# Optimization experiments

Hardware: AMD Instinct MI355X
Metric: run time of the kernel (lower is better)

The kernel has to match this reference:

```python
import jax, jax.numpy as jnp
import numpy as np

N_EMBD = 2048
N_HEAD = 16
HEAD_DIM = N_EMBD // N_HEAD
B, T = 4, 2048
EPS = 1e-5


def layer_norm(x, w, b):
    mu = jnp.mean(x, axis=-1, keepdims=True)
    var = jnp.var(x, axis=-1, keepdims=True)
    return (x - mu) * jax.lax.rsqrt(var + EPS) * w + b


def setup_inputs() -> dict:
    key = jax.random.key(0)
    ks = jax.random.split(key, 8)
    s = 0.02
    return {
        "x": jax.random.normal(ks[0], (B, T, N_EMBD), dtype=jnp.float32),
        "ln1_w": jnp.ones((N_EMBD,), jnp.float32),
        "ln1_b": jnp.zeros((N_EMBD,), jnp.float32),
        "attn_w": jax.random.normal(ks[1], (N_EMBD, 3 * N_EMBD), jnp.float32) * s,
        "attn_b": jnp.zeros((3 * N_EMBD,), jnp.float32),
        "ln2_w": jnp.ones((N_EMBD,), jnp.float32),
        "ln2_b": jnp.zeros((N_EMBD,), jnp.float32),
        "fc_w": jax.random.normal(ks[2], (N_EMBD, 4 * N_EMBD), jnp.float32) * s,
        "fc_b": jnp.zeros((4 * N_EMBD,), jnp.float32),
        "proj_w": jax.random.normal(ks[3], (4 * N_EMBD, N_EMBD), jnp.float32) * s,
        "proj_b": jnp.zeros((N_EMBD,), jnp.float32),
    }


def reference(x, ln1_w, ln1_b, attn_w, attn_b, ln2_w, ln2_b, fc_w, fc_b, proj_w, proj_b):
    b, t, c = x.shape
    # --- causal self-attention on ln_1(x); note: source Block has NO residual
    # and attention's c_proj is never invoked in the original forward. ---
    h = layer_norm(x, ln1_w, ln1_b)
    qkv = h @ attn_w + attn_b                      # [B,T,3C]
    q, k, v = jnp.split(qkv, 3, axis=-1)
    q = q.reshape(b, t, N_HEAD, HEAD_DIM)
    k = k.reshape(b, t, N_HEAD, HEAD_DIM)
    v = v.reshape(b, t, N_HEAD, HEAD_DIM)
    scale = 1.0 / np.sqrt(HEAD_DIM).astype(np.float32)
    scores = jnp.einsum("bqhd,bkhd->bhqk", q, k) * scale   # [B,H,T,T]
    causal = jnp.tril(jnp.ones((t, t), dtype=bool))
    scores = jnp.where(causal, scores, -jnp.inf)
    attn = jax.nn.softmax(scores, axis=-1)
    y = jnp.einsum("bhqk,bkhd->bqhd", attn, v).reshape(b, t, c)
    # --- MLP on ln_2(y); again no residual in the source Block ---
    h2 = layer_norm(y, ln2_w, ln2_b)
    out = jax.nn.gelu(h2 @ fc_w + fc_b, approximate=False) @ proj_w + proj_b
    return out
```

## Files before the change

kernel.cpp:

```cpp
#include <hip/hip_runtime.h>
#include <hip/hip_bf16.h>

typedef __attribute__((ext_vector_type(8))) short      bf16x8;
typedef __attribute__((ext_vector_type(4))) float      f32x4;
typedef __attribute__((ext_vector_type(8))) unsigned short u16x8;

__device__ __forceinline__ unsigned short f2bf(float f) {
    union { __hip_bfloat16 h; unsigned short u; } cv;
    cv.h = __float2bfloat16(f);
    return cv.u;
}
__device__ __forceinline__ float bf2f(unsigned short u) {
    union { float f; unsigned int i; } cv;
    cv.i = ((unsigned int)u) << 16;
    return cv.f;
}
__device__ __forceinline__ void gload_lds16(const void* g, void* l) {
    __builtin_amdgcn_global_load_lds(
        (const __attribute__((address_space(1))) void*)g,
        (__attribute__((address_space(3))) void*)l, 16, 0, 0);
}
__device__ __forceinline__ f32x4 mfma16(bf16x8 a, bf16x8 b, f32x4 c) {
    return __builtin_amdgcn_mfma_f32_16x16x32_bf16(a, b, c, 0, 0, 0);
}
__device__ __forceinline__ float gelu_f(float x) {
    return 0.5f * x * (1.0f + erff(x * 0.70710678118654752f));
}

#define S_BARRIER() asm volatile("s_barrier" ::: "memory")
#define LGKM0()     do { asm volatile("s_waitcnt lgkmcnt(0)" ::: "memory"); \
                         __builtin_amdgcn_sched_barrier(0); } while (0)

template<int IN_BF16>
__global__ __launch_bounds__(256) void ln_kernel(const void* in, const float* w, const float* b,
                                                 unsigned short* out) {
    const int row = blockIdx.x;
    const int tid = threadIdx.x;
    float v[8];
    if constexpr (IN_BF16) {
        const unsigned short* p = (const unsigned short*)in + (size_t)row * 2048 + tid * 8;
        u16x8 raw = *(const u16x8*)p;
#pragma unroll
        for (int j = 0; j < 8; j++) v[j] = bf2f(raw[j]);
    } else {
        const float* p = (const float*)in + (size_t)row * 2048 + tid * 8;
        float4 a = ((const float4*)p)[0];
        float4 c = ((const float4*)p)[1];
        v[0] = a.x; v[1] = a.y; v[2] = a.z; v[3] = a.w;
        v[4] = c.x; v[5] = c.y; v[6] = c.z; v[7] = c.w;
    }
    float s = 0.f, ss = 0.f;
#pragma unroll
    for (int j = 0; j < 8; j++) { s += v[j]; ss += v[j] * v[j]; }
#pragma unroll
    for (int off = 32; off > 0; off >>= 1) {
        s  += __shfl_xor(s, off);
        ss += __shfl_xor(ss, off);
    }
    __shared__ float red[8];
    const int wid = tid >> 6, lane = tid & 63;
    if (lane == 0) { red[wid] = s; red[4 + wid] = ss; }
    __syncthreads();
    s  = red[0] + red[1] + red[2] + red[3];
    ss = red[4] + red[5] + red[6] + red[7];
    const float mean = s * (1.0f / 2048.0f);
    const float var  = ss * (1.0f / 2048.0f) - mean * mean;
    const float rstd = rsqrtf(var + 1e-5f);
    unsigned short* op = out + (size_t)row * 2048 + tid * 8;
    u16x8 ov;
#pragma unroll
    for (int j = 0; j < 8; j++) {
        int c = tid * 8 + j;
        ov[j] = f2bf((v[j] - mean) * rstd * w[c] + b[c]);
    }
    *(u16x8*)op = ov;
}

__global__ __launch_bounds__(256) void wt_kernel(const float* W, unsigned short* WT, int K, int N) {
    __shared__ unsigned short sm[32][33];
    const int n0 = blockIdx.x * 32, k0 = blockIdx.y * 32;
    const int tx = threadIdx.x, ty = threadIdx.y;
#pragma unroll
    for (int i = 0; i < 4; i++) {
        int k = ty + i * 8;
        sm[k][tx] = f2bf(W[(size_t)(k0 + k) * N + n0 + tx]);
    }
    __syncthreads();
#pragma unroll
    for (int i = 0; i < 4; i++) {
        int n = ty + i * 8;
        WT[(size_t)(n0 + n) * K + k0 + tx] = sm[tx][n];
    }
}

__global__ __launch_bounds__(256) void vt_kernel(const unsigned short* qkv, unsigned short* vT) {
    __shared__ unsigned short sm[32][33];
    const int t0 = blockIdx.x * 32, d0 = blockIdx.y * 32, bh = blockIdx.z;
    const int b = bh >> 4, h = bh & 15;
    const int tx = threadIdx.x, ty = threadIdx.y;
#pragma unroll
    for (int i = 0; i < 4; i++) {
        int t = ty + i * 8;
        sm[t][tx] = qkv[(size_t)(b * 2048 + t0 + t) * 6144 + 4096 + h * 128 + d0 + tx];
    }
    __syncthreads();
#pragma unroll
    for (int i = 0; i < 4; i++) {
        int d = ty + i * 8;
        vT[(size_t)(bh * 128 + d0 + d) * 2048 + t0 + tx] = sm[tx][d];
    }
}

template<int OUT_BF16, int ACT_GELU>
__global__ __launch_bounds__(512, 2) void gemm256(const unsigned short* __restrict__ A,
                                                  const unsigned short* __restrict__ BT,
                                                  const float* __restrict__ bias,
                                                  void* __restrict__ Cout,
                                                  int M, int N, int K) {
    __shared__ unsigned short As[2][256 * 64];
    __shared__ unsigned short Bs[2][256 * 64];
    const int tid = threadIdx.x;
    const int gx = gridDim.x;
    const int lin = blockIdx.y * gx + blockIdx.x;
    const int cpx = (gx * gridDim.y) >> 3;
    const int swz = (lin & 7) * cpx + (lin >> 3);
    const int n0 = (swz % gx) * 256, m0 = (swz / gx) * 256;

    const int wid = tid >> 6, lane = tid & 63;
    const int wr = wid >> 2, wc = wid & 3;
    const int lg = lane >> 4, l15 = lane & 15;
    const int nkt = K >> 6;

    const int sr = tid >> 3;
    const int scol = ((tid & 7) ^ (sr & 7)) * 8;
    const int sdst = tid * 8;

    auto stageA = [&](int ta, int h) {
        const unsigned short* g = A + (size_t)(m0 + h * 128 + sr) * K + ta * 64 + scol;
        unsigned short* d = &As[ta & 1][h * 8192 + sdst];
        gload_lds16(g, d);
        gload_lds16(g + (size_t)64 * K, d + 4096);
    };
    auto stageB = [&](int ta, int h) {
        const unsigned short* g = BT + (size_t)(n0 + h * 128 + sr) * K + ta * 64 + scol;
        unsigned short* d = &Bs[ta & 1][h * 8192 + sdst];
        gload_lds16(g, d);
        gload_lds16(g + (size_t)64 * K, d + 4096);
    };

    stageA(0, 0); stageA(0, 1); stageB(0, 0); stageB(0, 1);
    if (nkt > 1) {
        stageA(1, 0); stageA(1, 1);
        asm volatile("s_waitcnt vmcnt(4)" ::: "memory");
    } else {
        asm volatile("s_waitcnt vmcnt(0)" ::: "memory");
    }
    S_BARRIER();

    f32x4 acc[8][4] = {};
    const int lxor = l15 & 7;
    const int co0 = (lg ^ lxor) * 8;
    const int co1 = ((4 + lg) ^ lxor) * 8;
    const int arow = wr * 128 + l15;
    const int brow = wc * 64 + l15;

    for (int t = 0; t < nkt; ++t) {
        const int p = t & 1;
        const unsigned short* Ap = As[p];
        const unsigned short* Bp = Bs[p];
        bf16x8 af0[8], af1[8], bq0, bq1;

#pragma unroll
        for (int m = 0; m < 8; m++) {
            const int rb = (arow + m * 16) * 64;
            af0[m] = *(const bf16x8*)&Ap[rb + co0];
            af1[m] = *(const bf16x8*)&Ap[rb + co1];
        }
        bq0 = *(const bf16x8*)&Bp[(brow) * 64 + co0];
        bq1 = *(const bf16x8*)&Bp[(brow + 16) * 64 + co0];
        if (t + 1 < nkt) { stageB(t + 1, 0); stageB(t + 1, 1); }
        S_BARRIER();
        LGKM0();
        __builtin_amdgcn_s_setprio(1);
#pragma unroll
        for (int m = 0; m < 8; m++) {
            acc[m][0] = mfma16(af0[m], bq0, acc[m][0]);
            acc[m][1] = mfma16(af0[m], bq1, acc[m][1]);
        }
        __builtin_amdgcn_s_setprio(0);
        S_BARRIER();

        bq0 = *(const bf16x8*)&Bp[(brow + 32) * 64 + co0];
        bq1 = *(const bf16x8*)&Bp[(brow + 48) * 64 + co0];
        if (t + 2 < nkt) stageA(t + 2, 0);
        S_BARRIER();
        LGKM0();
        __builtin_amdgcn_s_setprio(1);
#pragma unroll
        for (int m = 0; m < 8; m++) {
            acc[m][2] = mfma16(af0[m], bq0, acc[m][2]);
            acc[m][3] = mfma16(af0[m], bq1, acc[m][3]);
        }
        __builtin_amdgcn_s_setprio(0);
        S_BARRIER();

        bq0 = *(const bf16x8*)&Bp[(brow) * 64 + co1];
        bq1 = *(const bf16x8*)&Bp[(brow + 16) * 64 + co1];
        if (t + 2 < nkt) stageA(t + 2, 1);
        S_BARRIER();
        LGKM0();
        __builtin_amdgcn_s_setprio(1);
#pragma unroll
        for (int m = 0; m < 8; m++) {
            acc[m][0] = mfma16(af1[m], bq0, acc[m][0]);
            acc[m][1] = mfma16(af1[m], bq1, acc[m][1]);
        }
        __builtin_amdgcn_s_setprio(0);
        S_BARRIER();

        bq0 = *(const bf16x8*)&Bp[(brow + 32) * 64 + co1];
        bq1 = *(const bf16x8*)&Bp[(brow + 48) * 64 + co1];
        S_BARRIER();
        LGKM0();
        __builtin_amdgcn_s_setprio(1);
#pragma unroll
        for (int m = 0; m < 8; m++) {
            acc[m][2] = mfma16(af1[m], bq0, acc[m][2]);
            acc[m][3] = mfma16(af1[m], bq1, acc[m][3]);
        }
        __builtin_amdgcn_s_setprio(0);
        if (t + 2 < nkt)      asm volatile("s_waitcnt vmcnt(4)" ::: "memory");
        else if (t + 1 < nkt) asm volatile("s_waitcnt vmcnt(0)" ::: "memory");
        S_BARRIER();
    }

#pragma unroll
    for (int n = 0; n < 4; n++) {
        const int col = n0 + wc * 64 + n * 16 + l15;
        const float bv = bias[col];
#pragma unroll
        for (int m = 0; m < 8; m++) {
            const int rbase = m0 + wr * 128 + m * 16 + lg * 4;
#pragma unroll
            for (int r = 0; r < 4; r++) {
                float v = acc[m][n][r] + bv;
                if (ACT_GELU) v = gelu_f(v);
                if (OUT_BF16)
                    ((unsigned short*)Cout)[(size_t)(rbase + r) * N + col] = f2bf(v);
                else
                    ((float*)Cout)[(size_t)(rbase + r) * N + col] = v;
            }
        }
    }
}

__global__ __launch_bounds__(256) void attn_kernel(const unsigned short* __restrict__ qkv,
                                                   const unsigned short* __restrict__ vT,
                                                   unsigned short* __restrict__ y) {
    __shared__ unsigned short Qs[64 * 128];
    __shared__ unsigned short Ks[64 * 128];
    __shared__ unsigned short VTs[128 * 64];
    const int pair = blockIdx.x, h = blockIdx.y, b = blockIdx.z;
    const int tid = threadIdx.x, wid = tid >> 6, lane = tid & 63;
    const int lg = lane >> 4, l15 = lane & 15;
    const float scale = 0.08838834764831845f;
    unsigned short* Ps = &Qs[wid * 1024];

    for (int pass = 0; pass < 2; pass++) {
        const int qt = (pass == 0) ? (31 - pair) : pair;
        __syncthreads();
#pragma unroll
        for (int i = 0; i < 4; i++) {
            int idx = tid + 256 * i;
            int row = idx >> 4, ch = idx & 15;
            const unsigned short* g = qkv + (size_t)(b * 2048 + qt * 64 + row) * 6144
                                      + h * 128 + ((ch ^ (row & 7)) * 8);
            gload_lds16(g, &Qs[idx * 8]);
        }
        __syncthreads();
        const int rq = wid * 16 + l15;
        bf16x8 qf[4];
#pragma unroll
        for (int c = 0; c < 4; c++)
            qf[c] = *(const bf16x8*)&Qs[rq * 128 + (((c * 4 + lg) ^ (rq & 7)) * 8)];

        float m_run[4], l_run[4];
#pragma unroll
        for (int r = 0; r < 4; r++) { m_run[r] = -1e30f; l_run[r] = 0.f; }
        f32x4 O[8] = {};

        const int nkb = qt + 1;
        for (int kb = 0; kb < nkb; kb++) {
            __syncthreads();
#pragma unroll
            for (int i = 0; i < 4; i++) {
                int idx = tid + 256 * i;
                int row = idx >> 4, ch = idx & 15;
                const unsigned short* g = qkv + (size_t)(b * 2048 + kb * 64 + row) * 6144
                                          + 2048 + h * 128 + ((ch ^ (row & 7)) * 8);
                gload_lds16(g, &Ks[idx * 8]);
            }
#pragma unroll
            for (int i = 0; i < 4; i++) {
                int idx = tid + 256 * i;
                int row = idx >> 3, ch = idx & 7;
                const unsigned short* g = vT + (size_t)((b * 16 + h) * 128 + row) * 2048
                                          + kb * 64 + ((ch ^ (row & 7)) * 8);
                gload_lds16(g, &VTs[idx * 8]);
            }
            __syncthreads();

            f32x4 S[4] = {};
#pragma unroll
            for (int n = 0; n < 4; n++) {
                const int rk = n * 16 + l15;
#pragma unroll
                for (int c = 0; c < 4; c++) {
                    bf16x8 kf = *(const bf16x8*)&Ks[rk * 128 + (((c * 4 + lg) ^ (rk & 7)) * 8)];
                    S[n] = mfma16(qf[c], kf, S[n]);
                }
            }

            const int qgb = qt * 64 + wid * 16 + lg * 4;
#pragma unroll
            for (int r = 0; r < 4; r++) {
                const int qg = qgb + r;
                float sv[4];
#pragma unroll
                for (int n = 0; n < 4; n++) {
                    const int kg = kb * 64 + n * 16 + l15;
                    sv[n] = (kg <= qg) ? S[n][r] * scale : -1e30f;
                }
                float mx = fmaxf(fmaxf(sv[0], sv[1]), fmaxf(sv[2], sv[3]));
                mx = fmaxf(mx, __shfl_xor(mx, 1));
                mx = fmaxf(mx, __shfl_xor(mx, 2));
                mx = fmaxf(mx, __shfl_xor(mx, 4));
                mx = fmaxf(mx, __shfl_xor(mx, 8));
                const float mnew = fmaxf(m_run[r], mx);
                const float f = __expf(m_run[r] - mnew);
                const float p0 = __expf(sv[0] - mnew), p1 = __expf(sv[1] - mnew);
                const float p2 = __expf(sv[2] - mnew), p3 = __expf(sv[3] - mnew);
                float rs = (p0 + p1) + (p2 + p3);
                rs += __shfl_xor(rs, 1);
                rs += __shfl_xor(rs, 2);
                rs += __shfl_xor(rs, 4);
                rs += __shfl_xor(rs, 8);
                l_run[r] = l_run[r] * f + rs;
                m_run[r] = mnew;
#pragma unroll
                for (int n2 = 0; n2 < 8; n2++) O[n2][r] *= f;
                const int prow = lg * 4 + r;
                const int pxor = (prow & 7) << 3;
                Ps[(prow * 64 + l15) ^ pxor]      = f2bf(p0);
                Ps[(prow * 64 + 16 + l15) ^ pxor] = f2bf(p1);
                Ps[(prow * 64 + 32 + l15) ^ pxor] = f2bf(p2);
                Ps[(prow * 64 + 48 + l15) ^ pxor] = f2bf(p3);
            }

#pragma unroll
            for (int kk = 0; kk < 2; kk++) {
                bf16x8 pf = *(const bf16x8*)&Ps[l15 * 64 + (((kk * 4 + lg) ^ (l15 & 7)) * 8)];
#pragma unroll
                for (int n2 = 0; n2 < 8; n2++) {
                    const int rv = n2 * 16 + l15;
                    bf16x8 vf = *(const bf16x8*)&VTs[rv * 64 + (((kk * 4 + lg) ^ (rv & 7)) * 8)];
                    O[n2] = mfma16(pf, vf, O[n2]);
                }
            }
        }

#pragma unroll
        for (int r = 0; r < 4; r++) {
            const float inv = 1.0f / l_run[r];
            const size_t row = (size_t)(b * 2048 + qt * 64 + wid * 16 + lg * 4 + r);
#pragma unroll
            for (int n2 = 0; n2 < 8; n2++)
                y[row * 2048 + h * 128 + n2 * 16 + l15] = f2bf(O[n2][r] * inv);
        }
    }
}

extern "C" void kernel_launch(void* const* d_in, const int* in_sizes, int n_in,
                              void* d_out, int out_size, void* d_ws, size_t ws_size,
                              hipStream_t stream) {
    const float* x      = (const float*)d_in[0];
    const float* ln1_w  = (const float*)d_in[1];
    const float* ln1_b  = (const float*)d_in[2];
    const float* attn_w = (const float*)d_in[3];
    const float* attn_b = (const float*)d_in[4];
    const float* ln2_w  = (const float*)d_in[5];
    const float* ln2_b  = (const float*)d_in[6];
    const float* fc_w   = (const float*)d_in[7];
    const float* fc_b   = (const float*)d_in[8];
    const float* proj_w = (const float*)d_in[9];
    const float* proj_b = (const float*)d_in[10];
    float* out = (float*)d_out;

    char* ws = (char*)d_ws;
    const size_t MB = 1024ull * 1024ull;
    unsigned short* Wt   = (unsigned short*)(ws + 0);
    unsigned short* X1   = (unsigned short*)(ws + 32 * MB);
    unsigned short* X2   = (unsigned short*)(ws + 64 * MB);
    unsigned short* QKV  = (unsigned short*)(ws + 96 * MB);
    unsigned short* VT   = (unsigned short*)(ws + 192 * MB);
    unsigned short* Abuf = (unsigned short*)(ws + 96 * MB);

    ln_kernel<0><<<8192, 256, 0, stream>>>(x, ln1_w, ln1_b, X1);
    wt_kernel<<<dim3(6144 / 32, 2048 / 32), dim3(32, 8), 0, stream>>>(attn_w, Wt, 2048, 6144);
    gemm256<1, 0><<<dim3(24, 32), 512, 0, stream>>>(X1, Wt, attn_b, QKV, 8192, 6144, 2048);
    vt_kernel<<<dim3(64, 4, 64), dim3(32, 8), 0, stream>>>(QKV, VT);
    attn_kernel<<<dim3(16, 16, 4), 256, 0, stream>>>(QKV, VT, X2);
    ln_kernel<1><<<8192, 256, 0, stream>>>(X2, ln2_w, ln2_b, X1);
    wt_kernel<<<dim3(8192 / 32, 2048 / 32), dim3(32, 8), 0, stream>>>(fc_w, Wt, 2048, 8192);
    gemm256<1, 1><<<dim3(32, 32), 512, 0, stream>>>(X1, Wt, fc_b, Abuf, 8192, 8192, 2048);
    wt_kernel<<<dim3(2048 / 32, 8192 / 32), dim3(32, 8), 0, stream>>>(proj_w, Wt, 8192, 2048);
    gemm256<0, 0><<<dim3(8, 32), 512, 0, stream>>>(Abuf, Wt, proj_b, out, 8192, 2048, 8192);
}
```

Measured before the change: 1.045 ms.

## Restructure GEMM main loop into four half-M phases with one-tile-ahead prefetch

Rewrites the GEMM K-loop as four macro-generated phases. Each phase loads four A fragments and four B fragments and issues a 4x4 block of MFMAs, instead of holding all eight A fragments per K-half across the whole iteration. A and B are now both prefetched only one tile ahead, and the loop waits for all loads with vmcnt(0) at the end of each iteration. This is meant to cut register pressure and simplify the schedule, at the cost of a shallower prefetch that may expose more global-load latency.

After: 1.062 ms. Within noise of the previous version (+1.6%).

```diff
diff --git a/kernel.cpp b/kernel.cpp
--- a/kernel.cpp
+++ b/kernel.cpp
@@ -149,12 +149,7 @@
     };
 
     stageA(0, 0); stageA(0, 1); stageB(0, 0); stageB(0, 1);
-    if (nkt > 1) {
-        stageA(1, 0); stageA(1, 1);
-        asm volatile("s_waitcnt vmcnt(4)" ::: "memory");
-    } else {
-        asm volatile("s_waitcnt vmcnt(0)" ::: "memory");
-    }
+    asm volatile("s_waitcnt vmcnt(0)" ::: "memory");
     S_BARRIER();
 
     f32x4 acc[8][4] = {};
@@ -164,75 +159,49 @@
     const int arow = wr * 128 + l15;
     const int brow = wc * 64 + l15;
 
+#define GPHASE(MH, CO, READB, STAGE_STMT, TAIL_STMT)                              \
+    do {                                                                          \
+        bf16x8 af[4];                                                             \
+        _Pragma("unroll")                                                         \
+        for (int i = 0; i < 4; i++)                                               \
+            af[i] = *(const bf16x8*)&Ap[(arow + ((MH) * 4 + i) * 16) * 64 + (CO)];\
+        if (READB) {                                                              \
+            _Pragma("unroll")                                                     \
+            for (int n = 0; n < 4; n++)                                           \
+                bq[n] = *(const bf16x8*)&Bp[(brow + n * 16) * 64 + (CO)];         \
+        }                                                                         \
+        STAGE_STMT;                                                               \
+        S_BARRIER();                                                              \
+        LGKM0();                                                                  \
+        __builtin_amdgcn_s_setprio(1);                                            \
+        _Pragma("unroll")                                                         \
+        for (int i = 0; i < 4; i++) {                                             \
+            _Pragma("unroll")                                                     \
+            for (int n = 0; n < 4; n++)                                           \
+                acc[(MH) * 4 + i][n] = mfma16(af[i], bq[n], acc[(MH) * 4 + i][n]);\
+        }                                                                         \
+        __builtin_amdgcn_s_setprio(0);                                            \
+        TAIL_STMT;                                                                \
+        S_BARRIER();                                                              \
+    } while (0)
+
     for (int t = 0; t < nkt; ++t) {
         const int p = t & 1;
         const unsigned short* Ap = As[p];
         const unsigned short* Bp = Bs[p];
-        bf16x8 af0[8], af1[8], bq0, bq1;
-
-#pragma unroll
-        for (int m = 0; m < 8; m++) {
-            const int rb = (arow + m * 16) * 64;
-            af0[m] = *(const bf16x8*)&Ap[rb + co0];
-            af1[m] = *(const bf16x8*)&Ap[rb + co1];
-        }
-        bq0 = *(const bf16x8*)&Bp[(brow) * 64 + co0];
-        bq1 = *(const bf16x8*)&Bp[(brow + 16) * 64 + co0];
-        if (t + 1 < nkt) { stageB(t + 1, 0); stageB(t + 1, 1); }
-        S_BARRIER();
-        LGKM0();
-        __builtin_amdgcn_s_setprio(1);
-#pragma unroll
-        for (int m = 0; m < 8; m++) {
-            acc[m][0] = mfma16(af0[m], bq0, acc[m][0]);
-            acc[m][1] = mfma16(af0[m], bq1, acc[m][1]);
-        }
-        __builtin_amdgcn_s_setprio(0);
-        S_BARRIER();
-
-        bq0 = *(const bf16x8*)&Bp[(brow + 32) * 64 + co0];
-        bq1 = *(const bf16x8*)&Bp[(brow + 48) * 64 + co0];
-        if (t + 2 < nkt) stageA(t + 2, 0);
-        S_BARRIER();
-        LGKM0();
-        __builtin_amdgcn_s_setprio(1);
-#pragma unroll
-        for (int m = 0; m < 8; m++) {
-            acc[m][2] = mfma16(af0[m], bq0, acc[m][2]);
-            acc[m][3] = mfma16(af0[m], bq1, acc[m][3]);
-        }
-        __builtin_amdgcn_s_setprio(0);
-        S_BARRIER();
-
-        bq0 = *(const bf16x8*)&Bp[(brow) * 64 + co1];
-        bq1 = *(const bf16x8*)&Bp[(brow + 16) * 64 + co1];
-        if (t + 2 < nkt) stageA(t + 2, 1);
-        S_BARRIER();
-        LGKM0();
-        __builtin_amdgcn_s_setprio(1);
-#pragma unroll
-        for (int m = 0; m < 8; m++) {
-            acc[m][0] = mfma16(af1[m], bq0, acc[m][0]);
-            acc[m][1] = mfma16(af1[m], bq1, acc[m][1]);
-        }
-        __builtin_amdgcn_s_setprio(0);
-        S_BARRIER();
-
-        bq0 = *(const bf16x8*)&Bp[(brow + 32) * 64 + co1];
-        bq1 = *(const bf16x8*)&Bp[(brow + 48) * 64 + co1];
-        S_BARRIER();
-        LGKM0();
-        __builtin_amdgcn_s_setprio(1);
-#pragma unroll
-        for (int m = 0; m < 8; m++) {
-            acc[m][2] = mfma16(af1[m], bq0, acc[m][2]);
-            acc[m][3] = mfma16(af1[m], bq1, acc[m][3]);
-        }
-        __builtin_amdgcn_s_setprio(0);
-        if (t + 2 < nkt)      asm volatile("s_waitcnt vmcnt(4)" ::: "memory");
-        else if (t + 1 < nkt) asm volatile("s_waitcnt vmcnt(0)" ::: "memory");
-        S_BARRIER();
-    }
+        bf16x8 bq[4];
+
+        GPHASE(0, co0, 1,
+               if (t + 1 < nkt) { stageA(t + 1, 0); stageA(t + 1, 1); },
+               (void)0);
+        GPHASE(1, co0, 0,
+               if (t + 1 < nkt) { stageB(t + 1, 0); stageB(t + 1, 1); },
+               (void)0);
+        GPHASE(0, co1, 1, (void)0, (void)0);
+        GPHASE(1, co1, 0, (void)0,
+               if (t + 1 < nkt) asm volatile("s_waitcnt vmcnt(0)" ::: "memory"));
+    }
+#undef GPHASE
 
 #pragma unroll
     for (int n = 0; n < 4; n++) {
```
